# Performance work log

Measured on AMD Instinct MI355X. Metric: run time of the kernel, lower is better.

## Reference

```python
import jax, jax.numpy as jnp
import numpy as np

B, S, D = 64, 1452, 1024
G, K, R = 288, 4, 32
VIS = 1152  # number of vision patch tokens; tail is S - VIS = 300 text tokens
MAX_TOKENS = 300


def setup_inputs() -> dict:
    key = jax.random.key(0)
    k1, k2, k3, k4 = jax.random.split(key, 4)
    hidden_states = jax.random.normal(k1, (B, S, D), dtype=jnp.float32)
    attention_mask = jnp.ones((B, S), dtype=jnp.int32)
    # all batches share the same vision patch range [0, VIS-1]
    patch_range_list = jnp.tile(jnp.array([[0, VIS - 1]], dtype=jnp.int32), (B, 1))
    base = jnp.broadcast_to(jnp.arange(VIS, dtype=jnp.int32).reshape(1, G, K), (B, G, K))
    drop = jax.random.uniform(k2, (B, G, K)) < 0.1
    patch_indices_list_list = jnp.where(drop, jnp.int32(-1), base)
    rem = jax.random.randint(k3, (B, R), 0, VIS, dtype=jnp.int32)
    rem = jnp.where(jax.random.uniform(k4, (B, R)) < 0.25, jnp.int32(-1), rem)
    return {
        "hidden_states": hidden_states,
        "attention_mask": attention_mask,
        "patch_range_list": patch_range_list,
        "patch_indices_list_list": patch_indices_list_list,
        "remove_index_list_list": rem,
    }


def reference(hidden_states, attention_mask, patch_range_list, patch_indices_list_list, remove_index_list_list):
    Bn, Sn, Dn = hidden_states.shape
    _, Gn, Kn = patch_indices_list_list.shape
    # vision_end_token_index is taken from batch 0 in the original and used for a
    # shape-defining slice; treat as static (identical across batches here).
    vis_end = int(patch_range_list[0, 1]) + 1

    start = patch_range_list[:, 0]            # [B]
    end = patch_range_list[:, 1]              # [B]
    L = end - start + 1                       # [B] length of sliced hidden_state

    idx = patch_indices_list_list             # [B,G,K]
    mask = idx != -1                          # [B,G,K]
    # remove_index_list: drop -1 padding (map to -2 sentinel so it never matches)
    rem = jnp.where(remove_index_list_list == -1, jnp.int32(-2), remove_index_list_list)  # [B,R]
    in_rem = (idx[..., None] == rem[:, None, None, :]).any(-1)  # torch.isin, [B,G,K]
    mask = mask & ~in_rem

    # torch gather with -1 wraps to the last element of the SLICED hidden_state;
    # replicate exactly (note: the original sums wrapped/removed entries too).
    idx_w = jnp.where(idx >= 0, idx, idx + L[:, None, None])
    gidx = start[:, None, None] + idx_w       # absolute indices into hidden_states
    gathered = jnp.take_along_axis(
        hidden_states, gidx.reshape(Bn, Gn * Kn, 1), axis=1
    ).reshape(Bn, Gn, Kn, Dn)

    cnt = mask.sum(-1)                        # [B,G] divisor = count of kept entries
    pooled = gathered.sum(2) / jnp.maximum(cnt, 1)[..., None].astype(hidden_states.dtype)

    # rows with no valid entries are dropped; survivors are written right-aligned
    valid = mask.any(-1)                      # [B,G]
    n_valid = valid.sum(1)                    # [B]
    rank = jnp.cumsum(valid, axis=1) - 1      # 0-based rank among valid rows
    pos = jnp.where(valid, MAX_TOKENS - n_valid[:, None] + rank, MAX_TOKENS)  # OOB -> drop
    bidx = jnp.arange(Bn)[:, None]

    out_head = jnp.zeros((Bn, MAX_TOKENS, Dn), hidden_states.dtype).at[bidx, pos].set(pooled, mode="drop")
    att_head = jnp.zeros((Bn, MAX_TOKENS), attention_mask.dtype).at[bidx, pos].set(1, mode="drop")

    outputs = jnp.concatenate([out_head, hidden_states[:, vis_end:]], axis=1)
    outputs_attention = jnp.concatenate([att_head, attention_mask[:, vis_end:]], axis=1)
    return outputs, outputs_attention
```

## Files before the change

kernel.cpp:

```cpp
#include <hip/hip_runtime.h>
#include <hip/hip_bf16.h>

#define Bn 64
#define Sn 1452
#define Dn 1024
#define Gn 288
#define Kn 4
#define Rn 32
#define MAXT 300

typedef float f32x4 __attribute__((ext_vector_type(4)));

__global__ void __launch_bounds__(512)
phaseA_kernel(const int* __restrict__ idx,
              const int* __restrict__ rem,
              int* __restrict__ cnt_ws,
              int* __restrict__ gor_ws,
              int* __restrict__ nv_ws) {
    const int b = blockIdx.x;
    const int tid = threadIdx.x;

    __shared__ int s_rem[Rn];
    __shared__ int s_wsum[8];

    if (tid < Rn) {
        int r = rem[b * Rn + tid];
        s_rem[tid] = (r == -1) ? -2 : r;
    }
    __syncthreads();

    int cnt = 0;
    if (tid < Gn) {
#pragma unroll
        for (int k = 0; k < Kn; ++k) {
            int v = idx[(b * Gn + tid) * Kn + k];
            bool m = (v != -1);
            if (m) {
#pragma unroll
                for (int r = 0; r < Rn; ++r) {
                    if (v == s_rem[r]) { m = false; }
                }
            }
            cnt += m ? 1 : 0;
        }
        cnt_ws[b * Gn + tid] = cnt;
    }

    const int valid = (tid < Gn && cnt > 0) ? 1 : 0;
    const unsigned long long m = __ballot(valid);
    const int lane = tid & 63;
    const int w = tid >> 6;
    if (lane == 0) s_wsum[w] = __popcll(m);
    __syncthreads();

    int off = 0, tot = 0;
#pragma unroll
    for (int i = 0; i < 8; ++i) {
        int v = s_wsum[i];
        tot += v;
        if (i < w) off += v;
    }
    if (valid) {
        int rank = off + __popcll(m & ((1ull << lane) - 1ull));
        gor_ws[b * Gn + rank] = tid;
    }
    if (tid == 0) nv_ws[b] = tot;
}

__global__ void __launch_bounds__(256)
phaseB_kernel(const float* __restrict__ hs,
              const int* __restrict__ idx,
              const int* __restrict__ pr,
              const int* __restrict__ attn,
              const int* __restrict__ cnt_ws,
              const int* __restrict__ gor_ws,
              const int* __restrict__ nv_ws,
              float* __restrict__ out,
              float* __restrict__ att_out,
              int vis_end, int T) {
    const int t = blockIdx.x;
    const int b = blockIdx.y;
    const int tid = threadIdx.x;

    f32x4* outp = (f32x4*)(out + ((size_t)b * T + t) * Dn);

    if (t >= MAXT) {
        if (tid == 0)
            att_out[(size_t)b * T + t] = (float)attn[b * Sn + vis_end + (t - MAXT)];
        const f32x4* src = (const f32x4*)(hs + ((size_t)b * Sn + vis_end + (t - MAXT)) * Dn);
        __builtin_nontemporal_store(src[tid], &outp[tid]);
        return;
    }

    const int nvalid = nv_ws[b];
    if (tid == 0)
        att_out[(size_t)b * T + t] = (t >= MAXT - nvalid) ? 1.0f : 0.0f;

    if (t < MAXT - nvalid) {
        f32x4 z = {0.f, 0.f, 0.f, 0.f};
        __builtin_nontemporal_store(z, &outp[tid]);
        return;
    }

    const int g = gor_ws[b * Gn + (t - (MAXT - nvalid))];
    const int start = pr[b * 2];
    const int L = pr[b * 2 + 1] - start + 1;

    f32x4 acc = {0.f, 0.f, 0.f, 0.f};
#pragma unroll
    for (int k = 0; k < Kn; ++k) {
        int v = idx[(b * Gn + g) * Kn + k];
        int w = (v >= 0) ? v : v + L;
        const f32x4* row = (const f32x4*)(hs + ((size_t)b * Sn + start + w) * Dn);
        acc += row[tid];
    }
    const int c = cnt_ws[b * Gn + g];
    const float scale = 1.0f / (float)((c > 1) ? c : 1);
    acc *= scale;
    __builtin_nontemporal_store(acc, &outp[tid]);
}

extern "C" void kernel_launch(void* const* d_in, const int* in_sizes, int n_in,
                              void* d_out, int out_size, void* d_ws, size_t ws_size,
                              hipStream_t stream) {
    const float* hs  = (const float*)d_in[0];
    const int* attn  = (const int*)d_in[1];
    const int* pr    = (const int*)d_in[2];
    const int* idx   = (const int*)d_in[3];
    const int* rem   = (const int*)d_in[4];

    float* out = (float*)d_out;

    const int T = out_size / (Bn * (Dn + 1));
    const int vis_end = Sn - (T - MAXT);

    float* att_out = out + (size_t)Bn * T * Dn;

    int* cnt_ws = (int*)d_ws;
    int* gor_ws = cnt_ws + Bn * Gn;
    int* nv_ws  = gor_ws + Bn * Gn;

    phaseA_kernel<<<Bn, 512, 0, stream>>>(idx, rem, cnt_ws, gor_ws, nv_ws);
    phaseB_kernel<<<dim3(T, Bn), 256, 0, stream>>>(hs, idx, pr, attn,
                                                   cnt_ws, gor_ws, nv_ws,
                                                   out, att_out, vis_end, T);
}
```

Measured before the change: 95.05 us.

## Split tail copy into separate kernel and move attention-mask output to phase A

The combined per-row kernel is split into a head kernel (pooled rows and zero padding) and a tail kernel that copies the text-token rows in 16KB chunks, with each thread issuing four nontemporal loads before its stores. The attention-mask output is now written by the small phase-A kernel, so the big kernels no longer do scalar per-row writes. The aim is more memory-level parallelism for the tail copy and fewer divergent branches. It adds a third kernel launch on the same stream, and the tail copy no longer overlaps with phase A in any new way.

```diff
diff --git a/kernel.cpp b/kernel.cpp
--- a/kernel.cpp
+++ b/kernel.cpp
@@ -14,9 +14,12 @@
 __global__ void __launch_bounds__(512)
 phaseA_kernel(const int* __restrict__ idx,
               const int* __restrict__ rem,
+              const int* __restrict__ attn,
               int* __restrict__ cnt_ws,
               int* __restrict__ gor_ws,
-              int* __restrict__ nv_ws) {
+              int* __restrict__ nv_ws,
+              float* __restrict__ att_out,
+              int vis_end, int T) {
     const int b = blockIdx.x;
     const int tid = threadIdx.x;
 
@@ -65,37 +68,35 @@
         gor_ws[b * Gn + rank] = tid;
     }
     if (tid == 0) nv_ws[b] = tot;
+
+    const int nvalid = tot;
+    for (int t = tid; t < T; t += 512) {
+        float v;
+        if (t < MAXT) {
+            v = (t >= MAXT - nvalid) ? 1.0f : 0.0f;
+        } else {
+            v = (float)attn[b * Sn + vis_end + (t - MAXT)];
+        }
+        att_out[(size_t)b * T + t] = v;
+    }
 }
 
 __global__ void __launch_bounds__(256)
-phaseB_kernel(const float* __restrict__ hs,
-              const int* __restrict__ idx,
-              const int* __restrict__ pr,
-              const int* __restrict__ attn,
-              const int* __restrict__ cnt_ws,
-              const int* __restrict__ gor_ws,
-              const int* __restrict__ nv_ws,
-              float* __restrict__ out,
-              float* __restrict__ att_out,
-              int vis_end, int T) {
+head_kernel(const float* __restrict__ hs,
+            const int* __restrict__ idx,
+            const int* __restrict__ pr,
+            const int* __restrict__ cnt_ws,
+            const int* __restrict__ gor_ws,
+            const int* __restrict__ nv_ws,
+            float* __restrict__ out,
+            int T) {
     const int t = blockIdx.x;
     const int b = blockIdx.y;
     const int tid = threadIdx.x;
 
     f32x4* outp = (f32x4*)(out + ((size_t)b * T + t) * Dn);
 
-    if (t >= MAXT) {
-        if (tid == 0)
-            att_out[(size_t)b * T + t] = (float)attn[b * Sn + vis_end + (t - MAXT)];
-        const f32x4* src = (const f32x4*)(hs + ((size_t)b * Sn + vis_end + (t - MAXT)) * Dn);
-        __builtin_nontemporal_store(src[tid], &outp[tid]);
-        return;
-    }
-
     const int nvalid = nv_ws[b];
-    if (tid == 0)
-        att_out[(size_t)b * T + t] = (t >= MAXT - nvalid) ? 1.0f : 0.0f;
-
     if (t < MAXT - nvalid) {
         f32x4 z = {0.f, 0.f, 0.f, 0.f};
         __builtin_nontemporal_store(z, &outp[tid]);
@@ -120,6 +121,34 @@
     __builtin_nontemporal_store(acc, &outp[tid]);
 }
 
+__global__ void __launch_bounds__(256)
+tail_kernel(const float* __restrict__ hs,
+            float* __restrict__ out,
+            int vis_end, int T, int tail4) {
+    const int c = blockIdx.x;
+    const int b = blockIdx.y;
+    const int tid = threadIdx.x;
+
+    const f32x4* src = (const f32x4*)(hs + ((size_t)b * Sn + vis_end) * Dn);
+    f32x4* dst = (f32x4*)(out + ((size_t)b * T + MAXT) * Dn);
+
+    const int base = c * 1024;
+    f32x4 v0, v1, v2, v3;
+    int e0 = base + 0 * 256 + tid;
+    int e1 = base + 1 * 256 + tid;
+    int e2 = base + 2 * 256 + tid;
+    int e3 = base + 3 * 256 + tid;
+    bool p0 = e0 < tail4, p1 = e1 < tail4, p2 = e2 < tail4, p3 = e3 < tail4;
+    if (p0) v0 = __builtin_nontemporal_load(&src[e0]);
+    if (p1) v1 = __builtin_nontemporal_load(&src[e1]);
+    if (p2) v2 = __builtin_nontemporal_load(&src[e2]);
+    if (p3) v3 = __builtin_nontemporal_load(&src[e3]);
+    if (p0) __builtin_nontemporal_store(v0, &dst[e0]);
+    if (p1) __builtin_nontemporal_store(v1, &dst[e1]);
+    if (p2) __builtin_nontemporal_store(v2, &dst[e2]);
+    if (p3) __builtin_nontemporal_store(v3, &dst[e3]);
+}
+
 extern "C" void kernel_launch(void* const* d_in, const int* in_sizes, int n_in,
                               void* d_out, int out_size, void* d_ws, size_t ws_size,
                               hipStream_t stream) {
@@ -140,8 +169,13 @@
     int* gor_ws = cnt_ws + Bn * Gn;
     int* nv_ws  = gor_ws + Bn * Gn;
 
-    phaseA_kernel<<<Bn, 512, 0, stream>>>(idx, rem, cnt_ws, gor_ws, nv_ws);
-    phaseB_kernel<<<dim3(T, Bn), 256, 0, stream>>>(hs, idx, pr, attn,
-                                                   cnt_ws, gor_ws, nv_ws,
-                                                   out, att_out, vis_end, T);
+    const int tail_rows = T - MAXT;
+    const int tail4 = tail_rows * (Dn / 4);
+    const int nchunks = (tail_rows + 3) / 4;
+
+    phaseA_kernel<<<Bn, 512, 0, stream>>>(idx, rem, attn, cnt_ws, gor_ws, nv_ws,
+                                          att_out, vis_end, T);
+    tail_kernel<<<dim3(nchunks, Bn), 256, 0, stream>>>(hs, out, vis_end, T, tail4);
+    head_kernel<<<dim3(MAXT, Bn), 256, 0, stream>>>(hs, idx, pr, cnt_ws, gor_ws, nv_ws,
+                                                    out, T);
 }
```

After: 89.01 us. -6.4%, faster.
